# Kernel tuning notes

Hardware: AMD Instinct MI355X
Metric: run time of the kernel (lower is better)

## Reference

```python
import jax, jax.numpy as jnp
import numpy as np

NEG_INF = -1e30


def setup_inputs() -> dict:
    key = jax.random.key(0)
    kq, kk, kv, ks = jax.random.split(key, 4)
    B, H, S, D = 2, 16, 2048, 64
    return {
        "q": jax.random.normal(kq, (B, H, S, D), dtype=jnp.float32),
        "k": jax.random.normal(kk, (B, H, S, D), dtype=jnp.float32),
        "v": jax.random.normal(kv, (B, H, S, D), dtype=jnp.float32),
        "sink_weights": jax.random.normal(ks, (H,), dtype=jnp.float32),
        "sliding_window": 1024,
    }


def reference(q, k, v, sink_weights, sliding_window):
    """Sliding-window causal attention with a learnable attention-sink logit.

    Equivalent to FlexAttention.forward with sink_weights given: an extra kv
    position (the sink) is appended whose score is replaced by sink_weights[h]
    and whose value is zero -> it only adds mass to the softmax denominator.
    """
    B, H, S_q, D = q.shape
    S_kv = k.shape[2]
    scale = 1.0 / np.sqrt(D)

    # [B, H, S_q, S_kv] raw scores
    scores = jnp.einsum("bhqd,bhkd->bhqk", q, k) * scale

    q_idx = jnp.arange(S_q)[:, None]
    kv_idx = jnp.arange(S_kv)[None, :]
    keep = (kv_idx <= q_idx) & (q_idx - kv_idx <= sliding_window)  # [S_q, S_kv]
    scores = jnp.where(keep[None, None], scores, NEG_INF)

    # sink column: per-head learnable logit, always visible
    sink_col = jnp.broadcast_to(
        sink_weights[None, :, None, None], (B, H, S_q, 1)
    )
    logits = jnp.concatenate([scores, sink_col], axis=-1)  # [B,H,S_q,S_kv+1]

    probs = jax.nn.softmax(logits, axis=-1)
    # sink value is zero, so only the first S_kv prob columns hit v
    out = jnp.einsum("bhqk,bhkd->bhqd", probs[..., :S_kv], v)
    return out
```

## Files before the change

### kernel.cpp

```cpp
#include <hip/hip_runtime.h>


typedef __bf16 bf16x8 __attribute__((ext_vector_type(8)));
typedef __bf16 bf16x4 __attribute__((ext_vector_type(4)));
typedef float  f32x16 __attribute__((ext_vector_type(16)));

#define NT 256
#define NEG_BIG (-3.0e38f)

__device__ __forceinline__ int swz(int row, int gran) {
    return row * 64 + ((gran ^ ((row >> 1) & 7)) << 3);
}

__device__ const int SEG_N[24] = {3,2,2,2,2,1,2,1, 1,1,1,1,1,1,1,1, 1,1,1,1,1,1,1,1};
__device__ const int SEG_IT[24][3] = {
  {0,1,2},{2,3,0},{3,4,0},{4,5,0},{5,6,0},{6,0,0},{6,7,0},{7,0,0},
  {8,0,0},{8,0,0},{9,0,0},{9,0,0},{10,0,0},{10,0,0},{11,0,0},{11,0,0},
  {12,0,0},{12,0,0},{13,0,0},{13,0,0},{14,0,0},{14,0,0},{15,0,0},{15,0,0}};
__device__ const int SEG_J0[24][3] = {
  {0,0,0},{3,0,0},{6,0,0},{7,0,0},{6,0,0},{3,0,0},{12,0,0},{7,0,0},
  {0,0,0},{9,0,0},{0,0,0},{9,0,0},{0,0,0},{9,0,0},{0,0,0},{9,0,0},
  {0,0,0},{9,0,0},{0,0,0},{9,0,0},{0,0,0},{9,0,0},{0,0,0},{9,0,0}};
__device__ const int SEG_J1[24][3] = {
  {2,4,3},{6,6,0},{8,7,0},{10,6,0},{12,3,0},{12,0,0},{14,7,0},{16,0,0},
  {9,0,0},{18,0,0},{9,0,0},{18,0,0},{9,0,0},{18,0,0},{9,0,0},{18,0,0},
  {9,0,0},{18,0,0},{9,0,0},{18,0,0},{9,0,0},{18,0,0},{9,0,0},{18,0,0}};
__device__ const int SEG_SX[24][3] = {
  {0,0,0},{1,0,0},{1,0,0},{1,0,0},{1,0,0},{1,0,0},{2,0,0},{1,0,0},
  {0,0,0},{1,0,0},{0,0,0},{1,0,0},{0,0,0},{1,0,0},{0,0,0},{1,0,0},
  {0,0,0},{1,0,0},{0,0,0},{1,0,0},{0,0,0},{1,0,0},{0,0,0},{1,0,0}};
__device__ const int NSEG_ITEM[16] = {1,1,2,2,2,2,3,2, 2,2,2,2,2,2,2,2};

__global__ __launch_bounds__(NT, 3) void flex_r6_main(
    const float* __restrict__ Q, const float* __restrict__ K,
    const float* __restrict__ V, const float* __restrict__ SINKW,
    const int* __restrict__ SWIN, void* __restrict__ WS,
    float* __restrict__ OUT, const int H, const int S)
{
    const int t    = threadIdx.x;
    const int lane = t & 63;
    const int w    = t >> 6;
    const int c    = lane & 31;
    const int hl   = lane >> 5;
    const int W    = SWIN[0];
    const float scale = 0.125f;

    const int NBH = gridDim.x / 24;
    const int bh  = blockIdx.x / 24;
    const int b24 = blockIdx.x - bh * 24;
    const int h   = bh % H;
    const float sw = SINKW[h];

    __shared__ __align__(16) __bf16 k_lds[2][64 * 64];
    __shared__ __align__(16) __bf16 v_lds[2][64 * 64];
    __shared__ __align__(16) __bf16 p_lds[4][32 * 64];

    const size_t basebh = (size_t)bh * S * 64;
    const float4* kp4 = (const float4*)(K + basebh);
    const float4* vp4 = (const float4*)(V + basebh);
    __bf16* O_ws  = (__bf16*)WS;
    float2* ml_ws = (float2*)((char*)WS + (size_t)NBH * 48 * 16384);

    const int dgi = t & 15;
    const int kgi = t >> 4;
    float4 kreg[4], vreg[4];

    const int ns = SEG_N[b24];

    {
        const int it0 = SEG_IT[b24][0];
        const int ktA0 = (2 * it0 - 16 > 0) ? (2 * it0 - 16) : 0;
        const int kt = ktA0 + SEG_J0[b24][0];
        #pragma unroll
        for (int i = 0; i < 4; ++i) kreg[i] = kp4[kt * 1024 + i * NT + t];
        #pragma unroll
        for (int kk = 0; kk < 4; ++kk) vreg[kk] = vp4[kt * 1024 + (4 * kgi + kk) * 16 + dgi];
        #pragma unroll
        for (int i = 0; i < 4; ++i) {
            const int flat = i * NT + t;
            const int key = flat >> 4, dd = flat & 15;
            float4 f = kreg[i];
            bf16x4 b = { (__bf16)f.x, (__bf16)f.y, (__bf16)f.z, (__bf16)f.w };
            *(bf16x4*)&k_lds[0][swz(key, dd >> 1) + (dd & 1) * 4] = b;
        }
        {
            float4 a0 = vreg[0], a1 = vreg[1], a2 = vreg[2], a3 = vreg[3];
            bf16x4 w0 = { (__bf16)a0.x, (__bf16)a1.x, (__bf16)a2.x, (__bf16)a3.x };
            bf16x4 w1 = { (__bf16)a0.y, (__bf16)a1.y, (__bf16)a2.y, (__bf16)a3.y };
            bf16x4 w2 = { (__bf16)a0.z, (__bf16)a1.z, (__bf16)a2.z, (__bf16)a3.z };
            bf16x4 w3 = { (__bf16)a0.w, (__bf16)a1.w, (__bf16)a2.w, (__bf16)a3.w };
            const int gv = kgi >> 1, ov = (kgi & 1) * 4;
            *(bf16x4*)&v_lds[0][swz(4 * dgi + 0, gv) + ov] = w0;
            *(bf16x4*)&v_lds[0][swz(4 * dgi + 1, gv) + ov] = w1;
            *(bf16x4*)&v_lds[0][swz(4 * dgi + 2, gv) + ov] = w2;
            *(bf16x4*)&v_lds[0][swz(4 * dgi + 3, gv) + ov] = w3;
        }
    }

    int par = 0;

    for (int s = 0; s < ns; ++s) {
        const int item = SEG_IT[b24][s];
        const int j0   = SEG_J0[b24][s];
        const int j1   = SEG_J1[b24][s];
        const int sidx = SEG_SX[b24][s];
        const int ktA  = (2 * item - 16 > 0) ? (2 * item - 16) : 0;
        const int qw0  = item * 128 + 32 * w;
        const int qi   = qw0 + c;

        bf16x8 bq[4];
        {
            const float4* qp4 = (const float4*)(Q + basebh + (size_t)qi * 64);
            #pragma unroll
            for (int ks = 0; ks < 4; ++ks) {
                float4 f0 = qp4[4 * ks + 2 * hl];
                float4 f1 = qp4[4 * ks + 2 * hl + 1];
                bq[ks][0] = (__bf16)(f0.x * scale); bq[ks][1] = (__bf16)(f0.y * scale);
                bq[ks][2] = (__bf16)(f0.z * scale); bq[ks][3] = (__bf16)(f0.w * scale);
                bq[ks][4] = (__bf16)(f1.x * scale); bq[ks][5] = (__bf16)(f1.y * scale);
                bq[ks][6] = (__bf16)(f1.z * scale); bq[ks][7] = (__bf16)(f1.w * scale);
            }
        }

        float mrun = (sidx == 0) ? sw : NEG_BIG;
        float lrun = (sidx == 0) ? 1.0f : 0.0f;
        f32x16 accO0, accO1;
        #pragma unroll
        for (int i = 0; i < 16; ++i) { accO0[i] = 0.0f; accO1[i] = 0.0f; }

        for (int j = j0; j < j1; ++j) {
            const int k0 = (ktA + j) * 64;

            __syncthreads();

            int nkt = -1;
            if (j + 1 < j1) nkt = ktA + j + 1;
            else if (s + 1 < ns) {
                const int it2 = SEG_IT[b24][s + 1];
                const int ktA2 = (2 * it2 - 16 > 0) ? (2 * it2 - 16) : 0;
                nkt = ktA2 + SEG_J0[b24][s + 1];
            }
            if (nkt >= 0) {
                #pragma unroll
                for (int i = 0; i < 4; ++i) kreg[i] = kp4[nkt * 1024 + i * NT + t];
                #pragma unroll
                for (int kk = 0; kk < 4; ++kk) vreg[kk] = vp4[nkt * 1024 + (4 * kgi + kk) * 16 + dgi];
            }

            const __bf16* kb = k_lds[par];
            const __bf16* vb = v_lds[par];
            f32x16 accS0, accS1;
            #pragma unroll
            for (int i = 0; i < 16; ++i) { accS0[i] = 0.0f; accS1[i] = 0.0f; }
            #pragma unroll
            for (int ks = 0; ks < 4; ++ks) {
                bf16x8 ka0 = *(const bf16x8*)&kb[swz(c,      2 * ks + hl)];
                bf16x8 ka1 = *(const bf16x8*)&kb[swz(32 + c, 2 * ks + hl)];
                accS0 = __builtin_amdgcn_mfma_f32_32x32x16_bf16(ka0, bq[ks], accS0, 0, 0, 0);
                accS1 = __builtin_amdgcn_mfma_f32_32x32x16_bf16(ka1, bq[ks], accS1, 0, 0, 0);
            }

            const bool interior = (k0 + 63 <= qw0) && (qw0 + 31 - k0 <= W);
            if (!interior) {
                #pragma unroll
                for (int rg = 0; rg < 16; ++rg) {
                    const int kb2 = (rg & 3) + 8 * (rg >> 2) + 4 * hl;
                    const int ki0 = k0 + kb2, ki1 = k0 + 32 + kb2;
                    if (!((ki0 <= qi) && (qi - ki0 <= W))) accS0[rg] = -1e30f;
                    if (!((ki1 <= qi) && (qi - ki1 <= W))) accS1[rg] = -1e30f;
                }
            }

            float mx = accS0[0];
            #pragma unroll
            for (int i = 1; i < 16; ++i) mx = fmaxf(mx, accS0[i]);
            #pragma unroll
            for (int i = 0; i < 16; ++i) mx = fmaxf(mx, accS1[i]);
            mx = fmaxf(mx, __shfl_xor(mx, 32, 64));
            const float mnew  = fmaxf(mrun, mx);
            const float alpha = __expf(mrun - mnew);
            float ps = 0.0f;
            #pragma unroll
            for (int i = 0; i < 16; ++i) { float p = __expf(accS0[i] - mnew); accS0[i] = p; ps += p; }
            #pragma unroll
            for (int i = 0; i < 16; ++i) { float p = __expf(accS1[i] - mnew); accS1[i] = p; ps += p; }
            ps += __shfl_xor(ps, 32, 64);
            lrun = lrun * alpha + ps;
            mrun = mnew;
            #pragma unroll
            for (int i = 0; i < 16; ++i) { accO0[i] *= alpha; accO1[i] *= alpha; }

            __bf16* pw = p_lds[w];
            #pragma unroll
            for (int rg = 0; rg < 4; ++rg) {
                bf16x4 b0 = { (__bf16)accS0[4*rg+0], (__bf16)accS0[4*rg+1],
                              (__bf16)accS0[4*rg+2], (__bf16)accS0[4*rg+3] };
                bf16x4 b1 = { (__bf16)accS1[4*rg+0], (__bf16)accS1[4*rg+1],
                              (__bf16)accS1[4*rg+2], (__bf16)accS1[4*rg+3] };
                *(bf16x4*)&pw[swz(c, rg)     + 4 * hl] = b0;
                *(bf16x4*)&pw[swz(c, rg + 4) + 4 * hl] = b1;
            }

            #pragma unroll
            for (int ks = 0; ks < 4; ++ks) {
                bf16x8 bp  = *(const bf16x8*)&pw[swz(c, 2 * ks + hl)];
                bf16x8 va0 = *(const bf16x8*)&vb[swz(c,      2 * ks + hl)];
                bf16x8 va1 = *(const bf16x8*)&vb[swz(32 + c, 2 * ks + hl)];
                accO0 = __builtin_amdgcn_mfma_f32_32x32x16_bf16(va0, bp, accO0, 0, 0, 0);
                accO1 = __builtin_amdgcn_mfma_f32_32x32x16_bf16(va1, bp, accO1, 0, 0, 0);
            }

            if (nkt >= 0) {
                const int np = par ^ 1;
                #pragma unroll
                for (int i = 0; i < 4; ++i) {
                    const int flat = i * NT + t;
                    const int key = flat >> 4, dd = flat & 15;
                    float4 f = kreg[i];
                    bf16x4 b = { (__bf16)f.x, (__bf16)f.y, (__bf16)f.z, (__bf16)f.w };
                    *(bf16x4*)&k_lds[np][swz(key, dd >> 1) + (dd & 1) * 4] = b;
                }
                float4 a0 = vreg[0], a1 = vreg[1], a2 = vreg[2], a3 = vreg[3];
                bf16x4 w0 = { (__bf16)a0.x, (__bf16)a1.x, (__bf16)a2.x, (__bf16)a3.x };
                bf16x4 w1 = { (__bf16)a0.y, (__bf16)a1.y, (__bf16)a2.y, (__bf16)a3.y };
                bf16x4 w2 = { (__bf16)a0.z, (__bf16)a1.z, (__bf16)a2.z, (__bf16)a3.z };
                bf16x4 w3 = { (__bf16)a0.w, (__bf16)a1.w, (__bf16)a2.w, (__bf16)a3.w };
                const int gv = kgi >> 1, ov = (kgi & 1) * 4;
                *(bf16x4*)&v_lds[np][swz(4 * dgi + 0, gv) + ov] = w0;
                *(bf16x4*)&v_lds[np][swz(4 * dgi + 1, gv) + ov] = w1;
                *(bf16x4*)&v_lds[np][swz(4 * dgi + 2, gv) + ov] = w2;
                *(bf16x4*)&v_lds[np][swz(4 * dgi + 3, gv) + ov] = w3;
            }
            par ^= 1;
        }

        if (item < 2) {
            const float inv = 1.0f / lrun;
            float* ob = OUT + basebh + (size_t)qi * 64;
            #pragma unroll
            for (int rg = 0; rg < 4; ++rg) {
                float4 f0 = { accO0[4*rg+0]*inv, accO0[4*rg+1]*inv,
                              accO0[4*rg+2]*inv, accO0[4*rg+3]*inv };
                float4 f1 = { accO1[4*rg+0]*inv, accO1[4*rg+1]*inv,
                              accO1[4*rg+2]*inv, accO1[4*rg+3]*inv };
                *(float4*)&ob[     8 * rg + 4 * hl] = f0;
                *(float4*)&ob[32 + 8 * rg + 4 * hl] = f1;
            }
        } else {
            const int slot = (bh * 16 + item) * 3 + sidx;
            const int qrel = 32 * w + c;
            if (hl == 0) ml_ws[(size_t)slot * 128 + qrel] = make_float2(mrun, lrun);
            __bf16* Os = O_ws + (size_t)slot * 8192 + (size_t)qrel * 64;
            #pragma unroll
            for (int qd = 0; qd < 4; ++qd) {
                const int d0 = 8 * qd + 4 * hl;
                bf16x4 b0 = { (__bf16)accO0[4*qd+0], (__bf16)accO0[4*qd+1],
                              (__bf16)accO0[4*qd+2], (__bf16)accO0[4*qd+3] };
                bf16x4 b1 = { (__bf16)accO1[4*qd+0], (__bf16)accO1[4*qd+1],
                              (__bf16)accO1[4*qd+2], (__bf16)accO1[4*qd+3] };
                *(bf16x4*)&Os[d0]      = b0;
                *(bf16x4*)&Os[32 + d0] = b1;
            }
        }
    }
}

__global__ __launch_bounds__(256) void flex_r6_combine(
    const void* __restrict__ WS, float* __restrict__ OUT, const int H, const int S)
{
    const int NBH  = gridDim.x / 14;
    const int bi   = blockIdx.x;
    const int bh   = bi / 14;
    const int item = 2 + (bi - bh * 14);
    const int ns   = NSEG_ITEM[item];
    const int t    = threadIdx.x;
    const int q    = t >> 1;
    const int half = t & 1;

    const __bf16* O_ws = (const __bf16*)WS;
    const float2* ml_ws = (const float2*)((const char*)WS + (size_t)NBH * 48 * 16384);
    const int base = (bh * 16 + item) * 3;

    float m[3], lv[3], a[3];
    float mst = NEG_BIG;
    for (int s = 0; s < ns; ++s) {
        float2 e = ml_ws[(size_t)(base + s) * 128 + q];
        m[s] = e.x; lv[s] = e.y;
        mst = fmaxf(mst, m[s]);
    }
    float lst = 0.0f;
    for (int s = 0; s < ns; ++s) { a[s] = __expf(m[s] - mst); lst += a[s] * lv[s]; }
    const float inv = 1.0f / lst;

    float acc[32];
    #pragma unroll
    for (int i = 0; i < 32; ++i) acc[i] = 0.0f;
    for (int s = 0; s < ns; ++s) {
        const __bf16* Os = O_ws + (size_t)(base + s) * 8192 + (size_t)q * 64 + 32 * half;
        const float as = a[s];
        #pragma unroll
        for (int v8 = 0; v8 < 4; ++v8) {
            bf16x8 o = *(const bf16x8*)&Os[8 * v8];
            #pragma unroll
            for (int j = 0; j < 8; ++j) acc[8 * v8 + j] += as * (float)o[j];
        }
    }

    float* dst = OUT + (size_t)bh * S * 64 + (size_t)(item * 128 + q) * 64 + 32 * half;
    #pragma unroll
    for (int v4 = 0; v4 < 8; ++v4) {
        float4 f = { acc[4*v4+0] * inv, acc[4*v4+1] * inv,
                     acc[4*v4+2] * inv, acc[4*v4+3] * inv };
        *(float4*)&dst[4 * v4] = f;
    }
}

extern "C" void kernel_launch(void* const* d_in, const int* in_sizes, int n_in,
                              void* d_out, int out_size, void* d_ws, size_t ws_size,
                              hipStream_t stream) {
    const float* q     = (const float*)d_in[0];
    const float* k     = (const float*)d_in[1];
    const float* v     = (const float*)d_in[2];
    const float* sinkw = (const float*)d_in[3];
    const int*   swin  = (const int*)d_in[4];
    float* out = (float*)d_out;

    const int H = in_sizes[3];
    const int S = 2048;
    const int B = in_sizes[0] / (H * S * 64);
    const int NBH = B * H;

    flex_r6_main<<<dim3(NBH * 24), NT, 0, stream>>>(q, k, v, sinkw, swin, d_ws, out, H, S);
    flex_r6_combine<<<dim3(NBH * 14), 256, 0, stream>>>(d_ws, out, H, S);
}
```

Baseline: 140.0 us.

## Keep P in registers via lane swaps and rebalance work into 36 blocks per head

The softmax probability tile no longer goes through shared memory. It is now repacked in registers with cross-half-wave shuffles into the MFMA B-operand layout, which removes the P LDS writes and reads and the p_lds buffer. The split-KV schedule is rebuilt with 36 segments per batch-head instead of 24, using shorter chunks of 6 kv tiles, and launch bounds are raised to 4 blocks per CU. The aim is better load balance and occupancy, paid for with more partial outputs for the combine kernel to merge and higher register pressure.

```diff
diff --git a/kernel.cpp b/kernel.cpp
--- a/kernel.cpp
+++ b/kernel.cpp
@@ -12,26 +12,34 @@
     return row * 64 + ((gran ^ ((row >> 1) & 7)) << 3);
 }
 
-__device__ const int SEG_N[24] = {3,2,2,2,2,1,2,1, 1,1,1,1,1,1,1,1, 1,1,1,1,1,1,1,1};
-__device__ const int SEG_IT[24][3] = {
-  {0,1,2},{2,3,0},{3,4,0},{4,5,0},{5,6,0},{6,0,0},{6,7,0},{7,0,0},
-  {8,0,0},{8,0,0},{9,0,0},{9,0,0},{10,0,0},{10,0,0},{11,0,0},{11,0,0},
-  {12,0,0},{12,0,0},{13,0,0},{13,0,0},{14,0,0},{14,0,0},{15,0,0},{15,0,0}};
-__device__ const int SEG_J0[24][3] = {
-  {0,0,0},{3,0,0},{6,0,0},{7,0,0},{6,0,0},{3,0,0},{12,0,0},{7,0,0},
-  {0,0,0},{9,0,0},{0,0,0},{9,0,0},{0,0,0},{9,0,0},{0,0,0},{9,0,0},
-  {0,0,0},{9,0,0},{0,0,0},{9,0,0},{0,0,0},{9,0,0},{0,0,0},{9,0,0}};
-__device__ const int SEG_J1[24][3] = {
-  {2,4,3},{6,6,0},{8,7,0},{10,6,0},{12,3,0},{12,0,0},{14,7,0},{16,0,0},
-  {9,0,0},{18,0,0},{9,0,0},{18,0,0},{9,0,0},{18,0,0},{9,0,0},{18,0,0},
-  {9,0,0},{18,0,0},{9,0,0},{18,0,0},{9,0,0},{18,0,0},{9,0,0},{18,0,0}};
-__device__ const int SEG_SX[24][3] = {
-  {0,0,0},{1,0,0},{1,0,0},{1,0,0},{1,0,0},{1,0,0},{2,0,0},{1,0,0},
-  {0,0,0},{1,0,0},{0,0,0},{1,0,0},{0,0,0},{1,0,0},{0,0,0},{1,0,0},
-  {0,0,0},{1,0,0},{0,0,0},{1,0,0},{0,0,0},{1,0,0},{0,0,0},{1,0,0}};
-__device__ const int NSEG_ITEM[16] = {1,1,2,2,2,2,3,2, 2,2,2,2,2,2,2,2};
-
-__global__ __launch_bounds__(NT, 3) void flex_r6_main(
+__device__ __forceinline__ bf16x4 xswap32(bf16x4 v) {
+    union { bf16x4 v; int i[2]; } u;
+    u.v = v;
+    u.i[0] = __shfl_xor(u.i[0], 32, 64);
+    u.i[1] = __shfl_xor(u.i[1], 32, 64);
+    return u.v;
+}
+
+__device__ const int SEG_N[36]     = {2,1,1,2,1,1,1,1,1,2,1,1, 1,1,1,1,1,1,1,1,1,1,1,1,1,1,1,1,1,1,1,1,1,1,1,1};
+__device__ const int SEG_IT[36][2] = {
+  {0,1},{2,0},{3,0},{3,4},{4,0},{5,0},{5,0},{6,0},{6,0},{6,7},{7,0},{7,0},
+  {8,0},{8,0},{8,0},{9,0},{9,0},{9,0},{10,0},{10,0},{10,0},{11,0},{11,0},{11,0},
+  {12,0},{12,0},{12,0},{13,0},{13,0},{13,0},{14,0},{14,0},{14,0},{15,0},{15,0},{15,0}};
+__device__ const int SEG_J0[36][2] = {
+  {0,0},{0,0},{0,0},{6,0},{4,0},{0,0},{6,0},{0,0},{6,0},{12,0},{4,0},{10,0},
+  {0,0},{6,0},{12,0},{0,0},{6,0},{12,0},{0,0},{6,0},{12,0},{0,0},{6,0},{12,0},
+  {0,0},{6,0},{12,0},{0,0},{6,0},{12,0},{0,0},{6,0},{12,0},{0,0},{6,0},{12,0}};
+__device__ const int SEG_J1[36][2] = {
+  {2,4},{6,0},{6,0},{8,4},{10,0},{6,0},{12,0},{6,0},{12,0},{14,4},{10,0},{16,0},
+  {6,0},{12,0},{18,0},{6,0},{12,0},{18,0},{6,0},{12,0},{18,0},{6,0},{12,0},{18,0},
+  {6,0},{12,0},{18,0},{6,0},{12,0},{18,0},{6,0},{12,0},{18,0},{6,0},{12,0},{18,0}};
+__device__ const int SEG_SX[36][2] = {
+  {0,0},{0,0},{0,0},{1,0},{1,0},{0,0},{1,0},{0,0},{1,0},{2,0},{1,0},{2,0},
+  {0,0},{1,0},{2,0},{0,0},{1,0},{2,0},{0,0},{1,0},{2,0},{0,0},{1,0},{2,0},
+  {0,0},{1,0},{2,0},{0,0},{1,0},{2,0},{0,0},{1,0},{2,0},{0,0},{1,0},{2,0}};
+__device__ const int NSEG_ITEM[16] = {1,1,1,2,2,2,3,3, 3,3,3,3,3,3,3,3};
+
+__global__ __launch_bounds__(NT, 4) void flex_r7_main(
     const float* __restrict__ Q, const float* __restrict__ K,
     const float* __restrict__ V, const float* __restrict__ SINKW,
     const int* __restrict__ SWIN, void* __restrict__ WS,
@@ -45,15 +53,14 @@
     const int W    = SWIN[0];
     const float scale = 0.125f;
 
-    const int NBH = gridDim.x / 24;
-    const int bh  = blockIdx.x / 24;
-    const int b24 = blockIdx.x - bh * 24;
+    const int NBH = gridDim.x / 36;
+    const int bh  = blockIdx.x / 36;
+    const int b36 = blockIdx.x - bh * 36;
     const int h   = bh % H;
     const float sw = SINKW[h];
 
     __shared__ __align__(16) __bf16 k_lds[2][64 * 64];
     __shared__ __align__(16) __bf16 v_lds[2][64 * 64];
-    __shared__ __align__(16) __bf16 p_lds[4][32 * 64];
 
     const size_t basebh = (size_t)bh * S * 64;
     const float4* kp4 = (const float4*)(K + basebh);
@@ -65,12 +72,12 @@
     const int kgi = t >> 4;
     float4 kreg[4], vreg[4];
 
-    const int ns = SEG_N[b24];
+    const int ns = SEG_N[b36];
 
     {
-        const int it0 = SEG_IT[b24][0];
+        const int it0 = SEG_IT[b36][0];
         const int ktA0 = (2 * it0 - 16 > 0) ? (2 * it0 - 16) : 0;
-        const int kt = ktA0 + SEG_J0[b24][0];
+        const int kt = ktA0 + SEG_J0[b36][0];
         #pragma unroll
         for (int i = 0; i < 4; ++i) kreg[i] = kp4[kt * 1024 + i * NT + t];
         #pragma unroll
@@ -100,10 +107,10 @@
     int par = 0;
 
     for (int s = 0; s < ns; ++s) {
-        const int item = SEG_IT[b24][s];
-        const int j0   = SEG_J0[b24][s];
-        const int j1   = SEG_J1[b24][s];
-        const int sidx = SEG_SX[b24][s];
+        const int item = SEG_IT[b36][s];
+        const int j0   = SEG_J0[b36][s];
+        const int j1   = SEG_J1[b36][s];
+        const int sidx = SEG_SX[b36][s];
         const int ktA  = (2 * item - 16 > 0) ? (2 * item - 16) : 0;
         const int qw0  = item * 128 + 32 * w;
         const int qi   = qw0 + c;
@@ -136,9 +143,9 @@
             int nkt = -1;
             if (j + 1 < j1) nkt = ktA + j + 1;
             else if (s + 1 < ns) {
-                const int it2 = SEG_IT[b24][s + 1];
+                const int it2 = SEG_IT[b36][s + 1];
                 const int ktA2 = (2 * it2 - 16 > 0) ? (2 * it2 - 16) : 0;
-                nkt = ktA2 + SEG_J0[b24][s + 1];
+                nkt = ktA2 + SEG_J0[b36][s + 1];
             }
             if (nkt >= 0) {
                 #pragma unroll
@@ -190,24 +197,37 @@
             #pragma unroll
             for (int i = 0; i < 16; ++i) { accO0[i] *= alpha; accO1[i] *= alpha; }
 
-            __bf16* pw = p_lds[w];
-            #pragma unroll
-            for (int rg = 0; rg < 4; ++rg) {
-                bf16x4 b0 = { (__bf16)accS0[4*rg+0], (__bf16)accS0[4*rg+1],
-                              (__bf16)accS0[4*rg+2], (__bf16)accS0[4*rg+3] };
-                bf16x4 b1 = { (__bf16)accS1[4*rg+0], (__bf16)accS1[4*rg+1],
-                              (__bf16)accS1[4*rg+2], (__bf16)accS1[4*rg+3] };
-                *(bf16x4*)&pw[swz(c, rg)     + 4 * hl] = b0;
-                *(bf16x4*)&pw[swz(c, rg + 4) + 4 * hl] = b1;
+            bf16x4 qA = { (__bf16)accS0[0],  (__bf16)accS0[1],  (__bf16)accS0[2],  (__bf16)accS0[3]  };
+            bf16x4 qB = { (__bf16)accS0[4],  (__bf16)accS0[5],  (__bf16)accS0[6],  (__bf16)accS0[7]  };
+            bf16x4 qC = { (__bf16)accS0[8],  (__bf16)accS0[9],  (__bf16)accS0[10], (__bf16)accS0[11] };
+            bf16x4 qD = { (__bf16)accS0[12], (__bf16)accS0[13], (__bf16)accS0[14], (__bf16)accS0[15] };
+            bf16x4 qE = { (__bf16)accS1[0],  (__bf16)accS1[1],  (__bf16)accS1[2],  (__bf16)accS1[3]  };
+            bf16x4 qF = { (__bf16)accS1[4],  (__bf16)accS1[5],  (__bf16)accS1[6],  (__bf16)accS1[7]  };
+            bf16x4 qG = { (__bf16)accS1[8],  (__bf16)accS1[9],  (__bf16)accS1[10], (__bf16)accS1[11] };
+            bf16x4 qH = { (__bf16)accS1[12], (__bf16)accS1[13], (__bf16)accS1[14], (__bf16)accS1[15] };
+            bf16x4 r0 = xswap32(hl ? qA : qB);
+            bf16x4 r1 = xswap32(hl ? qC : qD);
+            bf16x4 r2 = xswap32(hl ? qE : qF);
+            bf16x4 r3 = xswap32(hl ? qG : qH);
+            bf16x4 lo0 = hl ? r0 : qA, hi0 = hl ? qB : r0;
+            bf16x4 lo1 = hl ? r1 : qC, hi1 = hl ? qD : r1;
+            bf16x4 lo2 = hl ? r2 : qE, hi2 = hl ? qF : r2;
+            bf16x4 lo3 = hl ? r3 : qG, hi3 = hl ? qH : r3;
+            bf16x8 bp[4];
+            #pragma unroll
+            for (int e = 0; e < 4; ++e) {
+                bp[0][e] = lo0[e]; bp[0][4+e] = hi0[e];
+                bp[1][e] = lo1[e]; bp[1][4+e] = hi1[e];
+                bp[2][e] = lo2[e]; bp[2][4+e] = hi2[e];
+                bp[3][e] = lo3[e]; bp[3][4+e] = hi3[e];
             }
 
             #pragma unroll
             for (int ks = 0; ks < 4; ++ks) {
-                bf16x8 bp  = *(const bf16x8*)&pw[swz(c, 2 * ks + hl)];
                 bf16x8 va0 = *(const bf16x8*)&vb[swz(c,      2 * ks + hl)];
                 bf16x8 va1 = *(const bf16x8*)&vb[swz(32 + c, 2 * ks + hl)];
-                accO0 = __builtin_amdgcn_mfma_f32_32x32x16_bf16(va0, bp, accO0, 0, 0, 0);
-                accO1 = __builtin_amdgcn_mfma_f32_32x32x16_bf16(va1, bp, accO1, 0, 0, 0);
+                accO0 = __builtin_amdgcn_mfma_f32_32x32x16_bf16(va0, bp[ks], accO0, 0, 0, 0);
+                accO1 = __builtin_amdgcn_mfma_f32_32x32x16_bf16(va1, bp[ks], accO1, 0, 0, 0);
             }
 
             if (nkt >= 0) {
@@ -234,7 +254,7 @@
             par ^= 1;
         }
 
-        if (item < 2) {
+        if (item < 3) {
             const float inv = 1.0f / lrun;
             float* ob = OUT + basebh + (size_t)qi * 64;
             #pragma unroll
@@ -265,13 +285,13 @@
     }
 }
 
-__global__ __launch_bounds__(256) void flex_r6_combine(
+__global__ __launch_bounds__(256) void flex_r7_combine(
     const void* __restrict__ WS, float* __restrict__ OUT, const int H, const int S)
 {
-    const int NBH  = gridDim.x / 14;
+    const int NBH  = gridDim.x / 13;
     const int bi   = blockIdx.x;
-    const int bh   = bi / 14;
-    const int item = 2 + (bi - bh * 14);
+    const int bh   = bi / 13;
+    const int item = 3 + (bi - bh * 13);
     const int ns   = NSEG_ITEM[item];
     const int t    = threadIdx.x;
     const int q    = t >> 1;
@@ -302,7 +322,7 @@
         for (int v8 = 0; v8 < 4; ++v8) {
             bf16x8 o = *(const bf16x8*)&Os[8 * v8];
             #pragma unroll
-            for (int j = 0; j < 8; ++j) acc[8 * v8 + j] += as * (float)o[j];
+            for (int jj = 0; jj < 8; ++jj) acc[8 * v8 + jj] += as * (float)o[jj];
         }
     }
 
@@ -330,6 +350,6 @@
     const int B = in_sizes[0] / (H * S * 64);
     const int NBH = B * H;
 
-    flex_r6_main<<<dim3(NBH * 24), NT, 0, stream>>>(q, k, v, sinkw, swin, d_ws, out, H, S);
-    flex_r6_combine<<<dim3(NBH * 14), 256, 0, stream>>>(d_ws, out, H, S);
-}
+    flex_r7_main<<<dim3(NBH * 36), NT, 0, stream>>>(q, k, v, sinkw, swin, d_ws, out, H, S);
+    flex_r7_combine<<<dim3(NBH * 13), 256, 0, stream>>>(d_ws, out, H, S);
+}
```

Result: slower. 185.5 us (+32.5%).
